# Kernel tuning notes

Hardware: AMD Instinct MI355X
Metric: run time of the kernel (lower is better)

The kernel has to match this reference:

```python
import jax, jax.numpy as jnp
import numpy as np
import itertools

B, G, FIN, T = 8, 2048, 32, 10
H = 64
DIM = 2
M = 5            # kernel_size per dim
K = M ** DIM     # 25 spline weights
E = 262144
N = B * G

_BITS = np.array(list(itertools.product([0, 1], repeat=DIM)), dtype=np.int32)  # [S, DIM]
_STRIDES = (M ** np.arange(DIM)).astype(np.int32)                              # [DIM]


def _spline_basis(edge_attr):
    """Degree-1 open B-spline basis. Returns basis [E,S] (float) and widx [E,S] (int)."""
    frac = edge_attr * (M - 1)                       # pseudo in [0,1] -> [0, M-1]
    k0 = jnp.clip(jnp.floor(frac), 0, M - 2)
    t = frac - k0                                    # [E, DIM]
    k0 = k0.astype(jnp.int32)
    bits = jnp.asarray(_BITS)                        # [S, DIM]
    tb = jnp.where(bits[None] == 1, t[:, None, :], 1.0 - t[:, None, :])  # [E,S,DIM]
    basis = jnp.prod(tb, axis=-1)                    # [E, S]
    widx = jnp.sum((k0[:, None, :] + bits[None]) * jnp.asarray(_STRIDES)[None, None, :], axis=-1)
    return basis, widx                               # widx: [E, S] in [0, K)


def _spline_conv(x, W, Wroot, b, src, dst, basis, widx):
    # x: [N, Fin]; W: [K, Fin, Fout]; Wroot: [Fin, Fout]; b: [Fout]
    xw = jnp.einsum('nf,kfo->nko', x, W)             # [N, K, Fout]
    g = xw[src[:, None], widx]                       # [E, S, Fout]
    msg = jnp.einsum('es,eso->eo', basis, g)         # [E, Fout]
    agg = jax.ops.segment_sum(msg, dst, num_segments=N)
    deg = jax.ops.segment_sum(jnp.ones((src.shape[0],), x.dtype), dst, num_segments=N)
    return agg / jnp.maximum(deg, 1.0)[:, None] + x @ Wroot + b


def setup_inputs() -> dict:
    key = jax.random.key(0)
    ks = jax.random.split(key, 20)
    inp = {
        'x': jax.random.normal(ks[0], (B, G, FIN, T), dtype=jnp.float32),
        'edge_index': jax.random.randint(ks[1], (2, E), 0, N, dtype=jnp.int64),
        'edge_attr': jax.random.uniform(ks[2], (E, DIM), dtype=jnp.float32),
    }
    names = ['xr', 'hr', 'xz', 'hz', 'xn']
    for i, nm in enumerate(names):
        fin = FIN if nm[0] == 'x' else H
        k1, k2, k3 = jax.random.split(ks[3 + i], 3)
        inp[f'W_{nm}'] = jax.random.normal(k1, (K, fin, H), dtype=jnp.float32) * 0.05
        inp[f'root_{nm}'] = jax.random.normal(k2, (fin, H), dtype=jnp.float32) * 0.05
        inp[f'b_{nm}'] = jax.random.normal(k3, (H,), dtype=jnp.float32) * 0.05
    return inp


def reference(x, edge_index, edge_attr,
              W_xr, root_xr, b_xr, W_hr, root_hr, b_hr,
              W_xz, root_xz, b_xz, W_hz, root_hz, b_hz,
              W_xn, root_xn, b_xn):
    src = edge_index[0].astype(jnp.int32)
    dst = edge_index[1].astype(jnp.int32)
    basis, widx = _spline_basis(edge_attr)  # shared across all 6 conv calls

    conv = lambda v, W, Wr, b: _spline_conv(v, W, Wr, b, src, dst, basis, widx)

    def cell(h, xt):
        hr = conv(h, W_hr, root_hr, b_hr)  # computed once, used in r and n (original calls it twice)
        r = jax.nn.sigmoid(conv(xt, W_xr, root_xr, b_xr) + hr)
        z = jax.nn.sigmoid(conv(xt, W_xz, root_xz, b_xz) + conv(h, W_hz, root_hz, b_hz))
        n = jnp.tanh(conv(xt, W_xn, root_xn, b_xn) + r * hr)
        h_new = (1.0 - z) * n + z * h
        return h_new, h_new

    xs = jnp.moveaxis(x, -1, 0).reshape(T, N, FIN)   # [T, N, Fin]
    h0 = jnp.zeros((N, H), x.dtype)
    h_last, hs = jax.lax.scan(cell, h0, xs)          # hs: [T, N, H]

    layer_output = jnp.transpose(hs.reshape(T, B, G, H), (1, 2, 3, 0))  # [B, G, H, T]
    last_state = h_last.reshape(1, B, G, H)
    return layer_output, last_state
```

## Files before the change

kernel.cpp:

```cpp
#include <hip/hip_runtime.h>
#include <hip/hip_bf16.h>
#include <hip/hip_fp16.h>

#define NNODE 16384
#define EDGES 262144
#define HOUT 64
#define TSTEPS 10
#define NKT_H 52
#define NKT_X 26

typedef __attribute__((ext_vector_type(8))) short bf16x8;
typedef __attribute__((ext_vector_type(4))) float f32x4;
typedef unsigned short u16;

__device__ __forceinline__ u16 f2b(float x) {
  __hip_bfloat16 b = __float2bfloat16(x);
  return *reinterpret_cast<const u16*>(&b);
}
__device__ __forceinline__ float b2f(u16 v) {
  union { unsigned u; float f; } c;
  c.u = ((unsigned)v) << 16;
  return c.f;
}


__global__ __launch_bounds__(256) void xpose_kernel(const float* __restrict__ x,
                                                    u16* __restrict__ xTb) {
  const int i = blockIdx.x * 256 + threadIdx.x;
  if (i >= NNODE * 32) return;
  const float* src = x + (size_t)i * TSTEPS;
  #pragma unroll
  for (int t = 0; t < TSTEPS; ++t)
    xTb[(size_t)t * NNODE * 32 + i] = f2b(src[t]);
}

__device__ __forceinline__ int cell_of(float a0, float a1, float4* b) {
  const float f0 = a0 * 4.f, f1 = a1 * 4.f;
  const float k0f = fminf(fmaxf(floorf(f0), 0.f), 3.f);
  const float k1f = fminf(fmaxf(floorf(f1), 0.f), 3.f);
  const float t0 = f0 - k0f, t1 = f1 - k1f;
  b->x = (1.f - t0) * (1.f - t1);
  b->y = (1.f - t0) * t1;
  b->z = t0 * (1.f - t1);
  b->w = t0 * t1;
  return (int)k0f + 4 * (int)k1f;
}

__global__ __launch_bounds__(256) void cellcount_kernel(const int* __restrict__ ei,
                                                        const float* __restrict__ ea,
                                                        int* __restrict__ cnt) {
  const int e = blockIdx.x * 256 + threadIdx.x;
  if (e >= EDGES) return;
  const int d = ei[EDGES + e];
  float4 b;
  const int cell = cell_of(ea[2 * e], ea[2 * e + 1], &b);
  atomicAdd(&cnt[d * 16 + cell], 1);
}

__global__ __launch_bounds__(256) void nodesum_kernel(const int* __restrict__ cnt,
                                                      int* __restrict__ degi) {
  const int d = blockIdx.x * 256 + threadIdx.x;
  if (d >= NNODE) return;
  int s = 0;
  #pragma unroll
  for (int c = 0; c < 16; ++c) s += cnt[d * 16 + c];
  degi[d] = s;
}

__global__ __launch_bounds__(1024) void scan_kernel(const int* __restrict__ degi,
                                                    int* __restrict__ rp,
                                                    float* __restrict__ deg_inv) {
  __shared__ int sh[1024];
  const int tid = threadIdx.x;
  const int base = tid * 16;
  int loc[16];
  int sum = 0;
  #pragma unroll
  for (int i = 0; i < 16; ++i) { loc[i] = degi[base + i]; sum += loc[i]; }
  sh[tid] = sum;
  __syncthreads();
  for (int off = 1; off < 1024; off <<= 1) {
    int v = 0;
    if (tid >= off) v = sh[tid - off];
    __syncthreads();
    if (tid >= off) sh[tid] += v;
    __syncthreads();
  }
  int ex = sh[tid] - sum;
  #pragma unroll
  for (int i = 0; i < 16; ++i) {
    rp[base + i] = ex;
    ex += loc[i];
    deg_inv[base + i] = 1.f / (float)max(loc[i], 1);
  }
  if (tid == 1023) rp[NNODE] = ex;
}

__global__ __launch_bounds__(256) void rp2_kernel(const int* __restrict__ rp,
                                                  const int* __restrict__ cnt,
                                                  int* __restrict__ rp2) {
  const int d = blockIdx.x * 256 + threadIdx.x;
  if (d >= NNODE) return;
  int base = rp[d];
  #pragma unroll
  for (int c = 0; c < 16; ++c) {
    rp2[d * 16 + c] = base;
    base += cnt[d * 16 + c];
  }
  if (d == NNODE - 1) rp2[NNODE * 16] = base;
}

__global__ __launch_bounds__(256) void scatter2_kernel(const int* __restrict__ ei,
                                                       const float* __restrict__ ea,
                                                       const int* __restrict__ rp2,
                                                       int* __restrict__ cursor2,
                                                       int* __restrict__ esrc,
                                                       float4* __restrict__ ebasis) {
  const int e = blockIdx.x * 256 + threadIdx.x;
  if (e >= EDGES) return;
  const int s = ei[e];
  const int d = ei[EDGES + e];
  float4 b;
  const int cell = cell_of(ea[2 * e], ea[2 * e + 1], &b);
  const int pos = rp2[d * 16 + cell] + atomicAdd(&cursor2[d * 16 + cell], 1);
  esrc[pos] = s;
  ebasis[pos] = b;
}

__global__ __launch_bounds__(256) void wprep_frag(const float* __restrict__ W,
                                                  const float* __restrict__ root,
                                                  u16* __restrict__ out,
                                                  int kspfin, int nkt) {
  const int K = nkt * 32;
  const int i = blockIdx.x * 256 + threadIdx.x;
  if (i >= 64 * K) return;
  const int o = i / K, k = i % K;
  const float v = (k < kspfin) ? W[(size_t)k * 64 + o]
                               : root[(size_t)(k - kspfin) * 64 + o];
  const int ot = o >> 4, kt = k >> 5;
  const int lif = (o & 15) + (((k & 31) >> 3) << 4);
  out[(((size_t)(ot * nkt + kt)) << 9) + lif * 8 + (k & 7)] = f2b(v);
}

#define SEC(K0, K1, BND)                                               \
  {                                                                    \
    const int eC = (BND);                                              \
    for (; e < eC; ++e) {                                              \
      const int sD = p.esrc[e + 3];                                    \
      const float4 b2 = p.ebasis[e + 2];                               \
      const float v2 = GATHER(sC);                                     \
      acc[(K0) + 5 * (K1)]     += b0.x * v0;                           \
      acc[(K0) + 5 * (K1) + 1] += b0.z * v0;                           \
      acc[(K0) + 5 * (K1) + 5] += b0.y * v0;                           \
      acc[(K0) + 5 * (K1) + 6] += b0.w * v0;                           \
      b0 = b1; b1 = b2; v0 = v1; v1 = v2; sC = sD;                     \
    }                                                                  \
  }

#define SEC_ALL                                                        \
  SEC(0, 0, q0.y) SEC(1, 0, q0.z) SEC(2, 0, q0.w) SEC(3, 0, q1.x)     \
  SEC(0, 1, q1.y) SEC(1, 1, q1.z) SEC(2, 1, q1.w) SEC(3, 1, q2.x)     \
  SEC(0, 2, q2.y) SEC(1, 2, q2.z) SEC(2, 2, q2.w) SEC(3, 2, q3.x)     \
  SEC(0, 3, q3.y) SEC(1, 3, q3.z) SEC(2, 3, q3.w) SEC(3, 3, eEnd)

#define SEC_PROLOGUE                                                   \
  const int4 q0 = *(const int4*)(p.rp2 + d * 16);                      \
  const int4 q1 = *(const int4*)(p.rp2 + d * 16 + 4);                  \
  const int4 q2 = *(const int4*)(p.rp2 + d * 16 + 8);                  \
  const int4 q3 = *(const int4*)(p.rp2 + d * 16 + 12);                 \
  const int eEnd = p.rp2[d * 16 + 16];                                 \
  int e = q0.x;                                                        \
  int sC;                                                              \
  float4 b0, b1;                                                       \
  float v0, v1;                                                        \
  {                                                                    \
    const int sA = p.esrc[e], sB = p.esrc[e + 1];                      \
    sC = p.esrc[e + 2];                                                \
    b0 = p.ebasis[e]; b1 = p.ebasis[e + 1];                            \
    v0 = GATHER(sA); v1 = GATHER(sB);                                  \
  }


struct HEP {
  const u16* h_curb;
  const int* rp2;
  const int* esrc;
  const float4* ebasis;
  const float* deg_inv;
  u16* Uh;
};

__global__ __launch_bounds__(256) void edge_h(HEP p) {
  const int wave = threadIdx.x >> 6, lane = threadIdx.x & 63;
  const int d = blockIdx.x * 4 + wave;
  float acc[25];
  #pragma unroll
  for (int k = 0; k < 25; ++k) acc[k] = 0.f;
  #define GATHER(S) b2f(p.h_curb[((S) << 6) + lane])
  SEC_PROLOGUE
  SEC_ALL
  #undef GATHER
  const float di = p.deg_inv[d];
  const int rt = d >> 4;
  const int lif8 = ((d & 15) + (((lane & 31) >> 3) << 4)) * 8 + (lane & 7);
  u16* ug = p.Uh + (((size_t)rt * NKT_H) << 9) + lif8;
  const int kth = lane >> 5;
  #pragma unroll
  for (int c = 0; c < 25; ++c)
    ug[(size_t)(2 * c + kth) << 9] = f2b(acc[c] * di);
  ug[(size_t)(50 + kth) << 9] = p.h_curb[(d << 6) + lane];
}

struct XEP {
  const u16* xTb;
  const int* rp2;
  const int* esrc;
  const float4* ebasis;
  const float* deg_inv;
  u16* Ux;
};

__global__ __launch_bounds__(256) void edge_x(XEP p, int tp) {
  const int wave = threadIdx.x >> 6, lane = threadIdx.x & 63;
  const int half = lane >> 5, fl = lane & 31;
  const int d = blockIdx.x * 4 + wave;
  const u16* __restrict__ xb = p.xTb + (size_t)(tp * 2 + half) * NNODE * 32;
  float acc[25];
  #pragma unroll
  for (int k = 0; k < 25; ++k) acc[k] = 0.f;
  #define GATHER(S) b2f(xb[((S) << 5) + fl])
  SEC_PROLOGUE
  SEC_ALL
  #undef GATHER
  const float di = p.deg_inv[d];
  const int rt = (half << 10) + (d >> 4);
  const int lif8 = ((d & 15) + ((fl >> 3) << 4)) * 8 + (fl & 7);
  u16* ug = p.Ux + (((size_t)rt * NKT_X) << 9) + lif8;
  #pragma unroll
  for (int c = 0; c < 25; ++c)
    ug[(size_t)c << 9] = f2b(acc[c] * di);
  ug[(size_t)25 << 9] = xb[(d << 5) + fl];
}


struct XGP {
  const u16* Ux;
  const u16* Wxfrag;
  const float* b_xr; const float* b_xz; const float* b_xn;
  __half* xcr; __half* xcz; __half* xcn;
};

__global__ __launch_bounds__(768) void gemm_x(XGP p, int tp) {
  const int tid = threadIdx.x;
  const int wave = tid >> 6, lane = tid & 63;
  const int g = wave >> 2, ot = wave & 3;
  const int col = lane & 15, q = lane >> 4;
  const int o = ot * 16 + col;
  const float* bp = (g == 0) ? p.b_xr : (g == 1) ? p.b_xz : p.b_xn;
  __half* outp = (g == 0) ? p.xcr : (g == 1) ? p.xcz : p.xcn;
  const float bias = bp[o];
  bf16x8 w[NKT_X];
  const u16* wf = p.Wxfrag + (((size_t)(g * 4 + ot) * NKT_X) << 9) + lane * 8;
  #pragma unroll
  for (int kt = 0; kt < NKT_X; ++kt)
    w[kt] = *reinterpret_cast<const bf16x8*>(wf + ((size_t)kt << 9));

  for (int rl = 0; rl < 8; ++rl) {
    const int rt = blockIdx.x * 8 + rl;
    const u16* ua = p.Ux + (((size_t)rt * NKT_X) << 9) + lane * 8;
    f32x4 acc = f32x4{bias, bias, bias, bias};
    #pragma unroll
    for (int kt = 0; kt < NKT_X; ++kt) {
      const bf16x8 a = *reinterpret_cast<const bf16x8*>(ua + ((size_t)kt << 9));
      acc = __builtin_amdgcn_mfma_f32_16x16x32_bf16(a, w[kt], acc, 0, 0, 0);
    }
    const int t = tp * 2 + (rt >> 10);
    const int nbase = (rt & 1023) << 4;
    #pragma unroll
    for (int j = 0; j < 4; ++j) {
      const int n = nbase + q * 4 + j;
      outp[((size_t)t * NNODE + n) * 64 + o] = __float2half(acc[j]);
    }
  }
}


struct HGP {
  const u16* Uh;
  const u16* Whfrag;
  const float* b_hr; const float* b_hz;
  const float* h_cur;
  float* h_next;
  u16* h_nextb;
  const __half* xcr; const __half* xcz; const __half* xcn;
  u16* hs;
};

__global__ __launch_bounds__(512) void gemm_h(HGP p, int t) {
  __shared__ __align__(16) float4 UA4[3328];
  const int tid = threadIdx.x;
  const int wave = tid >> 6, lane = tid & 63;
  const int rt = blockIdx.x;
  {
    const float4* src = (const float4*)(p.Uh + (((size_t)rt * NKT_H) << 9));
    for (int i = tid; i < 3328; i += 512) UA4[i] = src[i];
  }
  __syncthreads();

  const int g = wave & 1, ot = wave >> 1;
  const int col = lane & 15, q = lane >> 4;
  const int o = ot * 16 + col;
  const float bias = g ? p.b_hz[o] : p.b_hr[o];
  f32x4 acc = f32x4{bias, bias, bias, bias};
  const u16* ua = (const u16*)UA4 + lane * 8;
  const u16* wf = p.Whfrag + (((size_t)(g * 4 + ot) * NKT_H) << 9) + lane * 8;
  #pragma unroll 4
  for (int kt = 0; kt < NKT_H; ++kt) {
    const bf16x8 a = *reinterpret_cast<const bf16x8*>(ua + ((size_t)kt << 9));
    const bf16x8 w = *reinterpret_cast<const bf16x8*>(wf + ((size_t)kt << 9));
    acc = __builtin_amdgcn_mfma_f32_16x16x32_bf16(a, w, acc, 0, 0, 0);
  }
  __syncthreads();
  float* gates = (float*)UA4;
  #pragma unroll
  for (int j = 0; j < 4; ++j)
    gates[(g << 10) + (q * 4 + j) * 64 + o] = acc[j];
  __syncthreads();

  #pragma unroll
  for (int rep = 0; rep < 2; ++rep) {
    const int i = tid + rep * 512;
    const int nloc = i >> 6, oo = i & 63;
    const int node = (rt << 4) + nloc;
    const size_t idx = (size_t)node * 64 + oo;
    const size_t tix = (size_t)t * NNODE * 64 + idx;
    const float hrv = gates[nloc * 64 + oo];
    const float hzv = gates[1024 + nloc * 64 + oo];
    const float xrv = __half2float(p.xcr[tix]);
    const float xzv = __half2float(p.xcz[tix]);
    const float xnv = __half2float(p.xcn[tix]);
    const float r = 1.f / (1.f + __expf(-(xrv + hrv)));
    const float z = 1.f / (1.f + __expf(-(xzv + hzv)));
    const float ng = 1.f - 2.f / (__expf(2.f * (xnv + r * hrv)) + 1.f);
    const float hp = p.h_cur[idx];
    const float hn = (1.f - z) * ng + z * hp;
    p.h_next[idx] = hn;
    const u16 hb = f2b(hn);
    p.h_nextb[idx] = hb;
    p.hs[tix] = hb;
  }
}


__global__ __launch_bounds__(256) void finalize_kernel(const u16* __restrict__ hs,
                                                       float* __restrict__ out,
                                                       float* __restrict__ out_last) {
  const int i = blockIdx.x * 256 + threadIdx.x;
  if (i >= NNODE * 64) return;
  float* ob = out + (size_t)(i >> 6) * 640 + (size_t)(i & 63) * 10;
  #pragma unroll
  for (int t = 0; t < TSTEPS; ++t)
    ob[t] = b2f(hs[(size_t)t * NNODE * 64 + i]);
  out_last[i] = b2f(hs[(size_t)9 * NNODE * 64 + i]);
}


extern "C" void kernel_launch(void* const* d_in, const int* in_sizes, int n_in,
                              void* d_out, int out_size, void* d_ws, size_t ws_size,
                              hipStream_t stream) {
  const float* x = (const float*)d_in[0];
  const int* ei = (const int*)d_in[1];
  const float* ea = (const float*)d_in[2];
  const float* W_xr = (const float*)d_in[3];
  const float* root_xr = (const float*)d_in[4];
  const float* b_xr = (const float*)d_in[5];
  const float* W_hr = (const float*)d_in[6];
  const float* root_hr = (const float*)d_in[7];
  const float* b_hr = (const float*)d_in[8];
  const float* W_xz = (const float*)d_in[9];
  const float* root_xz = (const float*)d_in[10];
  const float* b_xz = (const float*)d_in[11];
  const float* W_hz = (const float*)d_in[12];
  const float* root_hz = (const float*)d_in[13];
  const float* b_hz = (const float*)d_in[14];
  const float* W_xn = (const float*)d_in[15];
  const float* root_xn = (const float*)d_in[16];
  const float* b_xn = (const float*)d_in[17];

  char* w = (char*)d_ws;
  u16* xTb = (u16*)w;          w += (size_t)TSTEPS * NNODE * 32 * 2;
  __half* xcr = (__half*)w;    w += (size_t)TSTEPS * NNODE * 64 * 2;
  __half* xcz = (__half*)w;    w += (size_t)TSTEPS * NNODE * 64 * 2;
  __half* xcn = (__half*)w;    w += (size_t)TSTEPS * NNODE * 64 * 2;
  u16* hs = (u16*)w;           w += (size_t)TSTEPS * NNODE * 64 * 2;
  float* h0 = (float*)w;       w += (size_t)NNODE * HOUT * 4;
  float* h1 = (float*)w;       w += (size_t)NNODE * HOUT * 4;
  u16* h0b = (u16*)w;          w += (size_t)NNODE * HOUT * 2;
  u16* h1b = (u16*)w;          w += (size_t)NNODE * HOUT * 2;
  float4* ebasis = (float4*)w; w += (size_t)(EDGES + 16) * 16;
  int* esrc = (int*)w;         w += (size_t)(EDGES + 16) * 4;
  u16* Whfrag = (u16*)w;       w += (size_t)2 * 4 * NKT_H * 512 * 2;
  u16* Wxfrag = (u16*)w;       w += (size_t)3 * 4 * NKT_X * 512 * 2;
  u16* Uh = (u16*)w;           w += (size_t)1024 * NKT_H * 512 * 2;
  u16* Ux = (u16*)w;           w += (size_t)2048 * NKT_X * 512 * 2;
  int* cnt = (int*)w;          w += (size_t)NNODE * 16 * 4;
  int* cursor2 = (int*)w;      w += (size_t)NNODE * 16 * 4;
  int* rp2 = (int*)w;          w += (size_t)(NNODE * 16 + 16) * 4;
  int* degi = (int*)w;         w += (size_t)NNODE * 4;
  int* rp = (int*)w;           w += (size_t)(NNODE + 4) * 4;
  float* deg_inv = (float*)w;  w += (size_t)NNODE * 4;

  hipMemsetAsync(cnt, 0, (size_t)NNODE * 16 * 4, stream);
  hipMemsetAsync(cursor2, 0, (size_t)NNODE * 16 * 4, stream);
  hipMemsetAsync(h0, 0, (size_t)NNODE * HOUT * 4, stream);
  hipMemsetAsync(h0b, 0, (size_t)NNODE * HOUT * 2, stream);
  hipMemsetAsync((void*)(ebasis + EDGES), 0, 16 * 16, stream);
  hipMemsetAsync(esrc + EDGES, 0, 16 * 4, stream);

  xpose_kernel<<<(NNODE * 32 + 255) / 256, 256, 0, stream>>>(x, xTb);
  cellcount_kernel<<<(EDGES + 255) / 256, 256, 0, stream>>>(ei, ea, cnt);
  nodesum_kernel<<<(NNODE + 255) / 256, 256, 0, stream>>>(cnt, degi);
  scan_kernel<<<1, 1024, 0, stream>>>(degi, rp, deg_inv);
  rp2_kernel<<<(NNODE + 255) / 256, 256, 0, stream>>>(rp, cnt, rp2);
  scatter2_kernel<<<(EDGES + 255) / 256, 256, 0, stream>>>(ei, ea, rp2, cursor2,
                                                           esrc, ebasis);
  const int gWH = (64 * NKT_H * 32 + 255) / 256;
  const int gWX = (64 * NKT_X * 32 + 255) / 256;
  wprep_frag<<<gWH, 256, 0, stream>>>(W_hr, root_hr, Whfrag, 1600, NKT_H);
  wprep_frag<<<gWH, 256, 0, stream>>>(W_hz, root_hz, Whfrag + (size_t)4 * NKT_H * 512, 1600, NKT_H);
  wprep_frag<<<gWX, 256, 0, stream>>>(W_xr, root_xr, Wxfrag, 800, NKT_X);
  wprep_frag<<<gWX, 256, 0, stream>>>(W_xz, root_xz, Wxfrag + (size_t)4 * NKT_X * 512, 800, NKT_X);
  wprep_frag<<<gWX, 256, 0, stream>>>(W_xn, root_xn, Wxfrag + (size_t)8 * NKT_X * 512, 800, NKT_X);

  XEP xe;
  xe.xTb = xTb; xe.rp2 = rp2; xe.esrc = esrc; xe.ebasis = ebasis;
  xe.deg_inv = deg_inv; xe.Ux = Ux;
  XGP xg;
  xg.Ux = Ux; xg.Wxfrag = Wxfrag;
  xg.b_xr = b_xr; xg.b_xz = b_xz; xg.b_xn = b_xn;
  xg.xcr = xcr; xg.xcz = xcz; xg.xcn = xcn;
  for (int tp = 0; tp < TSTEPS / 2; ++tp) {
    edge_x<<<NNODE / 4, 256, 0, stream>>>(xe, tp);
    gemm_x<<<256, 768, 0, stream>>>(xg, tp);
  }

  HEP he;
  he.rp2 = rp2; he.esrc = esrc; he.ebasis = ebasis;
  he.deg_inv = deg_inv; he.Uh = Uh;
  HGP hg;
  hg.Uh = Uh; hg.Whfrag = Whfrag;
  hg.b_hr = b_hr; hg.b_hz = b_hz;
  hg.xcr = xcr; hg.xcz = xcz; hg.xcn = xcn;
  hg.hs = hs;

  float* ha = h0; float* hb_ = h1;
  u16* hab = h0b; u16* hbb = h1b;
  for (int t = 0; t < TSTEPS; ++t) {
    he.h_curb = hab;
    edge_h<<<NNODE / 4, 256, 0, stream>>>(he);
    hg.h_cur = ha; hg.h_next = hb_; hg.h_nextb = hbb;
    gemm_h<<<NNODE / 16, 512, 0, stream>>>(hg, t);
    float* tf = ha; ha = hb_; hb_ = tf;
    u16* tb = hab; hab = hbb; hbb = tb;
  }

  float* out = (float*)d_out;
  float* out_last = out + (size_t)NNODE * HOUT * TSTEPS;
  finalize_kernel<<<(NNODE * 64 + 255) / 256, 256, 0, stream>>>(hs, out, out_last);
}
```

Before: 1.298 ms.

## Store edge aggregates node-contiguous and swizzle into LDS MFMA fragment layout in GEMMs

The edge kernels now write each node's 25 aggregated spline channels plus the self feature as one contiguous row, instead of scattering 2-byte stores into the MFMA fragment tile layout. The fragment rearrangement moves into the GEMM kernels: gemm_h reorders while staging into LDS, and gemm_x now stages each row tile through a new XOR-swizzled LDS buffer rather than reading fragments straight from global memory. The aim is coalesced edge-kernel stores and bank-conflict-free LDS fragment reads, at the cost of integer division in the staging loops and extra barriers and LDS traffic in gemm_x.

After: 1.695 ms. 30.6% more time.

```diff
diff --git a/kernel.cpp b/kernel.cpp
--- a/kernel.cpp
+++ b/kernel.cpp
@@ -201,14 +201,10 @@
   SEC_ALL
   #undef GATHER
   const float di = p.deg_inv[d];
-  const int rt = d >> 4;
-  const int lif8 = ((d & 15) + (((lane & 31) >> 3) << 4)) * 8 + (lane & 7);
-  u16* ug = p.Uh + (((size_t)rt * NKT_H) << 9) + lif8;
-  const int kth = lane >> 5;
-  #pragma unroll
-  for (int c = 0; c < 25; ++c)
-    ug[(size_t)(2 * c + kth) << 9] = f2b(acc[c] * di);
-  ug[(size_t)(50 + kth) << 9] = p.h_curb[(d << 6) + lane];
+  u16* un = p.Uh + (size_t)d * 1664 + lane;
+  #pragma unroll
+  for (int c = 0; c < 25; ++c) un[c * 64] = f2b(acc[c] * di);
+  un[25 * 64] = p.h_curb[(d << 6) + lane];
 }
 
 struct XEP {
@@ -233,13 +229,10 @@
   SEC_ALL
   #undef GATHER
   const float di = p.deg_inv[d];
-  const int rt = (half << 10) + (d >> 4);
-  const int lif8 = ((d & 15) + ((fl >> 3) << 4)) * 8 + (fl & 7);
-  u16* ug = p.Ux + (((size_t)rt * NKT_X) << 9) + lif8;
-  #pragma unroll
-  for (int c = 0; c < 25; ++c)
-    ug[(size_t)c << 9] = f2b(acc[c] * di);
-  ug[(size_t)25 << 9] = xb[(d << 5) + fl];
+  u16* un = p.Ux + (size_t)half * ((size_t)NNODE * 832) + (size_t)d * 832 + fl;
+  #pragma unroll
+  for (int c = 0; c < 25; ++c) un[c * 32] = f2b(acc[c] * di);
+  un[25 * 32] = xb[(d << 5) + fl];
 }
 
 
@@ -251,6 +244,7 @@
 };
 
 __global__ __launch_bounds__(768) void gemm_x(XGP p, int tp) {
+  __shared__ __align__(16) float4 UX4[1664];
   const int tid = threadIdx.x;
   const int wave = tid >> 6, lane = tid & 63;
   const int g = wave >> 2, ot = wave & 3;
@@ -267,11 +261,25 @@
 
   for (int rl = 0; rl < 8; ++rl) {
     const int rt = blockIdx.x * 8 + rl;
-    const u16* ua = p.Ux + (((size_t)rt * NKT_X) << 9) + lane * 8;
+    __syncthreads();
+    {
+      const float4* src = (const float4*)(
+          p.Ux + ((size_t)(rt >> 10) * NNODE + (size_t)((rt & 1023) << 4)) * 832);
+      for (int i = tid; i < 1664; i += 768) {
+        const float4 v = src[i];
+        const int node = i / 104;
+        const int r = i - node * 104;
+        const int c = r >> 2, g8 = r & 3;
+        UX4[c * 64 + ((node + (g8 << 4)) ^ (c & 7))] = v;
+      }
+    }
+    __syncthreads();
     f32x4 acc = f32x4{bias, bias, bias, bias};
-    #pragma unroll
+    const u16* ua = (const u16*)UX4;
+    #pragma unroll 2
     for (int kt = 0; kt < NKT_X; ++kt) {
-      const bf16x8 a = *reinterpret_cast<const bf16x8*>(ua + ((size_t)kt << 9));
+      const bf16x8 a = *reinterpret_cast<const bf16x8*>(
+          ua + (kt * 64 + (lane ^ (kt & 7))) * 8);
       acc = __builtin_amdgcn_mfma_f32_16x16x32_bf16(a, w[kt], acc, 0, 0, 0);
     }
     const int t = tp * 2 + (rt >> 10);
@@ -302,8 +310,16 @@
   const int wave = tid >> 6, lane = tid & 63;
   const int rt = blockIdx.x;
   {
-    const float4* src = (const float4*)(p.Uh + (((size_t)rt * NKT_H) << 9));
-    for (int i = tid; i < 3328; i += 512) UA4[i] = src[i];
+    const float4* src = (const float4*)(p.Uh + (size_t)rt * 26624);
+    for (int i = tid; i < 3328; i += 512) {
+      const float4 v = src[i];
+      const int node = i / 208;
+      const int r = i - node * 208;
+      const int c = r >> 3, g8 = r & 7;
+      const int kt = 2 * c + (g8 >> 2);
+      const int lif = node + ((g8 & 3) << 4);
+      UA4[kt * 64 + (lif ^ ((kt >> 1) & 7))] = v;
+    }
   }
   __syncthreads();
 
@@ -312,11 +328,12 @@
   const int o = ot * 16 + col;
   const float bias = g ? p.b_hz[o] : p.b_hr[o];
   f32x4 acc = f32x4{bias, bias, bias, bias};
-  const u16* ua = (const u16*)UA4 + lane * 8;
+  const u16* ua = (const u16*)UA4;
   const u16* wf = p.Whfrag + (((size_t)(g * 4 + ot) * NKT_H) << 9) + lane * 8;
   #pragma unroll 4
   for (int kt = 0; kt < NKT_H; ++kt) {
-    const bf16x8 a = *reinterpret_cast<const bf16x8*>(ua + ((size_t)kt << 9));
+    const bf16x8 a = *reinterpret_cast<const bf16x8*>(
+        ua + (kt * 64 + (lane ^ ((kt >> 1) & 7))) * 8);
     const bf16x8 w = *reinterpret_cast<const bf16x8*>(wf + ((size_t)kt << 9));
     acc = __builtin_amdgcn_mfma_f32_16x16x32_bf16(a, w, acc, 0, 0, 0);
   }
@@ -401,8 +418,8 @@
   int* esrc = (int*)w;         w += (size_t)(EDGES + 16) * 4;
   u16* Whfrag = (u16*)w;       w += (size_t)2 * 4 * NKT_H * 512 * 2;
   u16* Wxfrag = (u16*)w;       w += (size_t)3 * 4 * NKT_X * 512 * 2;
-  u16* Uh = (u16*)w;           w += (size_t)1024 * NKT_H * 512 * 2;
-  u16* Ux = (u16*)w;           w += (size_t)2048 * NKT_X * 512 * 2;
+  u16* Uh = (u16*)w;           w += (size_t)NNODE * 1664 * 2;
+  u16* Ux = (u16*)w;           w += (size_t)2 * NNODE * 832 * 2;
   int* cnt = (int*)w;          w += (size_t)NNODE * 16 * 4;
   int* cursor2 = (int*)w;      w += (size_t)NNODE * 16 * 4;
   int* rp2 = (int*)w;          w += (size_t)(NNODE * 16 + 16) * 4;
```
